# Performance work log

Hardware: AMD Instinct MI355X
Metric: run time of the kernel (lower is better)

Reference implementation:

```python
import jax, jax.numpy as jnp
import numpy as np

B, T, E = 32, 2048, 1024

def setup_inputs() -> dict:
    key = jax.random.key(0)
    k1, k2, k3 = jax.random.split(key, 3)
    enc = jax.random.normal(k1, (B, T, E), dtype=jnp.float32)
    ctx = jax.random.normal(k2, (B, E), dtype=jnp.float32)
    W = jax.random.normal(k3, (E, E), dtype=jnp.float32) * 0.05
    b = jnp.zeros((1, E), dtype=jnp.float32)
    return {"enc": enc, "ctx": ctx, "W": W, "b": b}

def reference(enc, ctx, W, b):
    # ht: (B, T, E) = tanh(enc @ W + b)
    ht = jnp.tanh(jnp.einsum('bte,ef->btf', enc, W) + b)
    # scores: (B, T) = batch dot of ctx against each timestep of ht
    scores = jnp.einsum('be,bte->bt', ctx, ht)
    at = jax.nn.softmax(scores, axis=-1)
    # weighted sum pooling over time -> (B, E)
    return jnp.einsum('bt,bte->be', at, ht)
```

## Files before the change

kernel.cpp:

```cpp
#include <hip/hip_runtime.h>
#include <hip/hip_bf16.h>
#include <math.h>

typedef unsigned short u16;
typedef unsigned int   u32;
typedef _Float16 f16x8 __attribute__((ext_vector_type(8)));
typedef float f32x4  __attribute__((ext_vector_type(4)));

#define Bb 32
#define Tt 2048
#define Ee 1024
#define Mm (Bb*Tt)
#define LSTR 40

__device__ __forceinline__ float tanh_fast(float x) {
  float ax = fminf(fabsf(x), 15.0f);
  float e  = __expf(2.0f * ax);
  float t  = 1.0f - 2.0f / (e + 1.0f);
  return copysignf(t, x);
}

__device__ __forceinline__ u32 pack2h(float a, float b) {
  _Float16 ha = (_Float16)a, hb = (_Float16)b;
  return (u32)__builtin_bit_cast(u16, ha) | ((u32)__builtin_bit_cast(u16, hb) << 16);
}

__global__ __launch_bounds__(256) void wt_convert(const float* __restrict__ W,
                                                  u16* __restrict__ Wt_hi,
                                                  u16* __restrict__ Wt_lo) {
  __shared__ float tile[32][33];
  int n0 = blockIdx.x * 32, k0 = blockIdx.y * 32;
  int tx = threadIdx.x, ty = threadIdx.y;
#pragma unroll
  for (int i = 0; i < 4; ++i)
    tile[ty + 8*i][tx] = W[(size_t)(k0 + ty + 8*i) * Ee + n0 + tx];
  __syncthreads();
#pragma unroll
  for (int i = 0; i < 4; ++i) {
    float v = tile[tx][ty + 8*i];
    _Float16 hi = (_Float16)v;
    float rem = v - (float)hi;
    _Float16 lo = (_Float16)rem;
    size_t idx = (size_t)(n0 + ty + 8*i) * Ee + k0 + tx;
    Wt_hi[idx] = __builtin_bit_cast(u16, hi);
    Wt_lo[idx] = __builtin_bit_cast(u16, lo);
  }
}

__global__ __launch_bounds__(256, 2) void gemm_tanh_score(
    const float* __restrict__ enc, const float* __restrict__ ctx,
    const float* __restrict__ bias,
    const u16* __restrict__ Wt_hi, const u16* __restrict__ Wt_lo,
    u16* __restrict__ ht, float* __restrict__ scores) {
  __shared__ u16 Ahf[128*LSTR], Bhi[128*LSTR], Blo[128*LSTR];

  int bx = blockIdx.x;
  int nt = bx & 7, mt = bx >> 3;
  int m0 = mt * 128, n0 = nt * 128;
  int tid = threadIdx.x;
  int w = tid >> 6, lane = tid & 63;
  int wm = (w & 1) * 64, wn = (w >> 1) * 64;
  int q = lane >> 4, c = lane & 15;

  f32x4 zero = {0.f, 0.f, 0.f, 0.f};
  f32x4 acc[4][4];
#pragma unroll
  for (int i = 0; i < 4; ++i)
#pragma unroll
    for (int j = 0; j < 4; ++j) acc[i][j] = zero;

  int ar = tid >> 1, ah = tid & 1;
  const float* Ap  = enc   + (size_t)(m0 + ar) * Ee + ah * 16;
  const u16*   BhP = Wt_hi + (size_t)(n0 + ar) * Ee + ah * 16;
  const u16*   BlP = Wt_lo + (size_t)(n0 + ar) * Ee + ah * 16;
  u16* AW  = &Ahf[ar * LSTR + ah * 16];
  u16* BhW = &Bhi[ar * LSTR + ah * 16];
  u16* BlW = &Blo[ar * LSTR + ah * 16];

  for (int kt = 0; kt < 32; ++kt) {
    const float4* ap = (const float4*)(Ap + (size_t)kt * 32);
    float4 f0 = ap[0], f1 = ap[1], f2 = ap[2], f3 = ap[3];
    const uint4* bhp = (const uint4*)(BhP + (size_t)kt * 32);
    uint4 bH0 = bhp[0], bH1 = bhp[1];
    const uint4* blp = (const uint4*)(BlP + (size_t)kt * 32);
    uint4 bL0 = blp[0], bL1 = blp[1];

    u32 a01 = pack2h(f0.x, f0.y), a23 = pack2h(f0.z, f0.w);
    u32 a45 = pack2h(f1.x, f1.y), a67 = pack2h(f1.z, f1.w);
    u32 a89 = pack2h(f2.x, f2.y), aAB = pack2h(f2.z, f2.w);
    u32 aCD = pack2h(f3.x, f3.y), aEF = pack2h(f3.z, f3.w);

    __syncthreads();
    ((uint4*)AW)[0]  = make_uint4(a01, a23, a45, a67);
    ((uint4*)AW)[1]  = make_uint4(a89, aAB, aCD, aEF);
    ((uint4*)BhW)[0] = bH0; ((uint4*)BhW)[1] = bH1;
    ((uint4*)BlW)[0] = bL0; ((uint4*)BlW)[1] = bL1;
    __syncthreads();

    f16x8 aF[4], bH[4], bL[4];
#pragma unroll
    for (int i = 0; i < 4; ++i) {
      int rax = (wm + i * 16 + c) * LSTR + q * 8;
      aF[i] = *(const f16x8*)(&Ahf[rax]);
      int rbx = (wn + i * 16 + c) * LSTR + q * 8;
      bH[i] = *(const f16x8*)(&Bhi[rbx]);
      bL[i] = *(const f16x8*)(&Blo[rbx]);
    }
#pragma unroll
    for (int i = 0; i < 4; ++i)
#pragma unroll
      for (int j = 0; j < 4; ++j) {
        acc[i][j] = __builtin_amdgcn_mfma_f32_16x16x32_f16(aF[i], bH[j], acc[i][j], 0, 0, 0);
        acc[i][j] = __builtin_amdgcn_mfma_f32_16x16x32_f16(aF[i], bL[j], acc[i][j], 0, 0, 0);
      }
  }

  int bidx = m0 >> 11;
  float ctxv[4], biasv[4];
#pragma unroll
  for (int j = 0; j < 4; ++j) {
    int col = n0 + wn + j * 16 + c;
    ctxv[j]  = ctx[bidx * Ee + col];
    biasv[j] = bias[col];
  }
#pragma unroll
  for (int i = 0; i < 4; ++i) {
#pragma unroll
    for (int r = 0; r < 4; ++r) {
      int rowG = m0 + wm + i * 16 + q * 4 + r;
      u16* hrow = ht + (size_t)rowG * Ee + n0 + wn + c;
      float s = 0.f;
#pragma unroll
      for (int j = 0; j < 4; ++j) {
        float h = tanh_fast(acc[i][j][r] + biasv[j]);
        __hip_bfloat16 hb = __float2bfloat16(h);
        hrow[j * 16] = *(u16*)&hb;
        s += h * ctxv[j];
      }
      s += __shfl_xor(s, 1); s += __shfl_xor(s, 2);
      s += __shfl_xor(s, 4); s += __shfl_xor(s, 8);
      if (c == 0) atomicAdd(&scores[rowG], s);
    }
  }
}

__global__ __launch_bounds__(256) void softmax_t(const float* __restrict__ scores,
                                                 float* __restrict__ at) {
  __shared__ float red[256];
  int b = blockIdx.x, tid = threadIdx.x;
  float v[8];
  float mx = -3.0e38f;
#pragma unroll
  for (int i = 0; i < 8; ++i) {
    v[i] = scores[b * Tt + i * 256 + tid];
    mx = fmaxf(mx, v[i]);
  }
  red[tid] = mx; __syncthreads();
  for (int s = 128; s > 0; s >>= 1) {
    if (tid < s) red[tid] = fmaxf(red[tid], red[tid + s]);
    __syncthreads();
  }
  mx = red[0]; __syncthreads();
  float sum = 0.f;
#pragma unroll
  for (int i = 0; i < 8; ++i) { v[i] = __expf(v[i] - mx); sum += v[i]; }
  red[tid] = sum; __syncthreads();
  for (int s = 128; s > 0; s >>= 1) {
    if (tid < s) red[tid] += red[tid + s];
    __syncthreads();
  }
  float inv = 1.0f / red[0];
#pragma unroll
  for (int i = 0; i < 8; ++i) at[b * Tt + i * 256 + tid] = v[i] * inv;
}

__global__ __launch_bounds__(256) void weighted_sum(const u16* __restrict__ ht,
                                                    const float* __restrict__ at,
                                                    float* __restrict__ part) {
  __shared__ float ats[64];
  int bx = blockIdx.x;
  int b = bx >> 5, tc = bx & 31;
  int tid = threadIdx.x;
  if (tid < 64) ats[tid] = at[b * Tt + tc * 64 + tid];
  __syncthreads();
  int e0 = tid * 4;
  const u16* base = ht + (size_t)(b * Tt + tc * 64) * Ee + e0;
  float s0 = 0.f, s1 = 0.f, s2 = 0.f, s3 = 0.f;
#pragma unroll 4
  for (int t = 0; t < 64; ++t) {
    float a = ats[t];
    uint2 u = *(const uint2*)(base + (size_t)t * Ee);
    s0 += a * __uint_as_float(u.x << 16);
    s1 += a * __uint_as_float(u.x & 0xffff0000u);
    s2 += a * __uint_as_float(u.y << 16);
    s3 += a * __uint_as_float(u.y & 0xffff0000u);
  }
  float4 out4 = make_float4(s0, s1, s2, s3);
  *(float4*)(part + ((size_t)(b * 32 + tc) * Ee + e0)) = out4;
}

__global__ __launch_bounds__(256) void reduce_part(const float* __restrict__ part,
                                                   float* __restrict__ out) {
  int b = blockIdx.x, tid = threadIdx.x;
  float4 s = make_float4(0.f, 0.f, 0.f, 0.f);
#pragma unroll
  for (int tc = 0; tc < 32; ++tc) {
    float4 p = ((const float4*)(part + (size_t)(b * 32 + tc) * Ee))[tid];
    s.x += p.x; s.y += p.y; s.z += p.z; s.w += p.w;
  }
  ((float4*)(out + (size_t)b * Ee))[tid] = s;
}

extern "C" void kernel_launch(void* const* d_in, const int* in_sizes, int n_in,
                              void* d_out, int out_size, void* d_ws, size_t ws_size,
                              hipStream_t stream) {
  const float* enc  = (const float*)d_in[0];
  const float* ctx  = (const float*)d_in[1];
  const float* W    = (const float*)d_in[2];
  const float* bias = (const float*)d_in[3];
  float* out = (float*)d_out;

  char* ws = (char*)d_ws;
  u16* Wt_hi = (u16*)(ws);
  u16* Wt_lo = (u16*)(ws + (size_t)2 * 1024 * 1024);
  u16* ht    = (u16*)(ws + (size_t)4 * 1024 * 1024);
  float* scores = (float*)(ws + (size_t)4 * 1024 * 1024 + (size_t)Mm * Ee * 2);
  float* at     = scores + Mm;
  float* part   = (float*)ws;

  hipMemsetAsync(scores, 0, (size_t)Mm * sizeof(float), stream);

  wt_convert<<<dim3(32, 32), dim3(32, 8), 0, stream>>>(W, Wt_hi, Wt_lo);
  gemm_tanh_score<<<dim3(4096), dim3(256), 0, stream>>>(enc, ctx, bias, Wt_hi, Wt_lo, ht, scores);
  softmax_t<<<dim3(32), dim3(256), 0, stream>>>(scores, at);
  weighted_sum<<<dim3(1024), dim3(256), 0, stream>>>(ht, at, part);
  reduce_part<<<dim3(32), dim3(256), 0, stream>>>(part, out);
}
```

Measured before the change: 716.5 us.

## Prefetch next K-tile into registers, swizzle block order, store ht as fp16

The GEMM main loop now loads the next K-tile of enc and W halves into registers right after the shared-memory store, so global latency overlaps the MFMA work on the current tile. Block indices are remapped so groups of 8 consecutive blocks cover different M tiles across all N tiles, which changes L2 reuse of enc and W. The ht intermediate moves from bf16 to fp16, giving it more mantissa precision at the cost of a smaller range, though tanh output stays within [-1,1]. The register prefetch raises register pressure under launch_bounds(256,2).

```diff
diff --git a/kernel.cpp b/kernel.cpp
--- a/kernel.cpp
+++ b/kernel.cpp
@@ -55,7 +55,9 @@
   __shared__ u16 Ahf[128*LSTR], Bhi[128*LSTR], Blo[128*LSTR];
 
   int bx = blockIdx.x;
-  int nt = bx & 7, mt = bx >> 3;
+  int x = bx & 7, local = bx >> 3;
+  int nt = local & 7;
+  int mt = ((local >> 3) << 3) + x;
   int m0 = mt * 128, n0 = nt * 128;
   int tid = threadIdx.x;
   int w = tid >> 6, lane = tid & 63;
@@ -77,25 +79,39 @@
   u16* BhW = &Bhi[ar * LSTR + ah * 16];
   u16* BlW = &Blo[ar * LSTR + ah * 16];
 
+  float4 fA0, fA1, fA2, fA3;
+  uint4 vH0, vH1, vL0, vL1;
+  {
+    const float4* ap = (const float4*)Ap;
+    fA0 = ap[0]; fA1 = ap[1]; fA2 = ap[2]; fA3 = ap[3];
+    const uint4* bhp = (const uint4*)BhP;
+    vH0 = bhp[0]; vH1 = bhp[1];
+    const uint4* blp = (const uint4*)BlP;
+    vL0 = blp[0]; vL1 = blp[1];
+  }
+
   for (int kt = 0; kt < 32; ++kt) {
-    const float4* ap = (const float4*)(Ap + (size_t)kt * 32);
-    float4 f0 = ap[0], f1 = ap[1], f2 = ap[2], f3 = ap[3];
-    const uint4* bhp = (const uint4*)(BhP + (size_t)kt * 32);
-    uint4 bH0 = bhp[0], bH1 = bhp[1];
-    const uint4* blp = (const uint4*)(BlP + (size_t)kt * 32);
-    uint4 bL0 = blp[0], bL1 = blp[1];
-
-    u32 a01 = pack2h(f0.x, f0.y), a23 = pack2h(f0.z, f0.w);
-    u32 a45 = pack2h(f1.x, f1.y), a67 = pack2h(f1.z, f1.w);
-    u32 a89 = pack2h(f2.x, f2.y), aAB = pack2h(f2.z, f2.w);
-    u32 aCD = pack2h(f3.x, f3.y), aEF = pack2h(f3.z, f3.w);
+    u32 a01 = pack2h(fA0.x, fA0.y), a23 = pack2h(fA0.z, fA0.w);
+    u32 a45 = pack2h(fA1.x, fA1.y), a67 = pack2h(fA1.z, fA1.w);
+    u32 a89 = pack2h(fA2.x, fA2.y), aAB = pack2h(fA2.z, fA2.w);
+    u32 aCD = pack2h(fA3.x, fA3.y), aEF = pack2h(fA3.z, fA3.w);
 
     __syncthreads();
     ((uint4*)AW)[0]  = make_uint4(a01, a23, a45, a67);
     ((uint4*)AW)[1]  = make_uint4(a89, aAB, aCD, aEF);
-    ((uint4*)BhW)[0] = bH0; ((uint4*)BhW)[1] = bH1;
-    ((uint4*)BlW)[0] = bL0; ((uint4*)BlW)[1] = bL1;
-    __syncthreads();
+    ((uint4*)BhW)[0] = vH0; ((uint4*)BhW)[1] = vH1;
+    ((uint4*)BlW)[0] = vL0; ((uint4*)BlW)[1] = vL1;
+    __syncthreads();
+
+    {
+      int kt2 = (kt < 31) ? kt + 1 : 31;
+      const float4* ap = (const float4*)(Ap + (size_t)kt2 * 32);
+      fA0 = ap[0]; fA1 = ap[1]; fA2 = ap[2]; fA3 = ap[3];
+      const uint4* bhp = (const uint4*)(BhP + (size_t)kt2 * 32);
+      vH0 = bhp[0]; vH1 = bhp[1];
+      const uint4* blp = (const uint4*)(BlP + (size_t)kt2 * 32);
+      vL0 = blp[0]; vL1 = blp[1];
+    }
 
     f16x8 aF[4], bH[4], bL[4];
 #pragma unroll
@@ -133,8 +149,8 @@
 #pragma unroll
       for (int j = 0; j < 4; ++j) {
         float h = tanh_fast(acc[i][j][r] + biasv[j]);
-        __hip_bfloat16 hb = __float2bfloat16(h);
-        hrow[j * 16] = *(u16*)&hb;
+        _Float16 hf = (_Float16)h;
+        hrow[j * 16] = __builtin_bit_cast(u16, hf);
         s += h * ctxv[j];
       }
       s += __shfl_xor(s, 1); s += __shfl_xor(s, 2);
@@ -190,10 +206,10 @@
   for (int t = 0; t < 64; ++t) {
     float a = ats[t];
     uint2 u = *(const uint2*)(base + (size_t)t * Ee);
-    s0 += a * __uint_as_float(u.x << 16);
-    s1 += a * __uint_as_float(u.x & 0xffff0000u);
-    s2 += a * __uint_as_float(u.y << 16);
-    s3 += a * __uint_as_float(u.y & 0xffff0000u);
+    s0 += a * (float)__builtin_bit_cast(_Float16, (u16)(u.x & 0xffff));
+    s1 += a * (float)__builtin_bit_cast(_Float16, (u16)(u.x >> 16));
+    s2 += a * (float)__builtin_bit_cast(_Float16, (u16)(u.y & 0xffff));
+    s3 += a * (float)__builtin_bit_cast(_Float16, (u16)(u.y >> 16));
   }
   float4 out4 = make_float4(s0, s1, s2, s3);
   *(float4*)(part + ((size_t)(b * 32 + tc) * Ee + e0)) = out4;
```

After: 730.1 us. About the same (+1.9%).

## Pre-convert enc to fp16 and stream GEMM tiles via direct global-to-LDS loads

Applied to the files above, without the earlier changes.

Adds a separate pass that converts enc to fp16 in workspace. The GEMM then fills its LDS tiles with global_load_lds DMA instead of register staging and conversion, using unpadded 32-wide rows. Block indices are also swizzled so neighbouring blocks share enc rows for L2 reuse, and ht is stored as fp16 instead of bf16. The trade is an extra full read and write of enc (256MB fp32 in, 128MB fp16 out) against fewer GEMM instructions and registers; unpadded LDS rows risk bank conflicts. The old path is kept when the workspace is too small.

```diff
diff --git a/kernel.cpp b/kernel.cpp
--- a/kernel.cpp
+++ b/kernel.cpp
@@ -11,7 +11,6 @@
 #define Tt 2048
 #define Ee 1024
 #define Mm (Bb*Tt)
-#define LSTR 40
 
 __device__ __forceinline__ float tanh_fast(float x) {
   float ax = fminf(fabsf(x), 15.0f);
@@ -23,6 +22,27 @@
 __device__ __forceinline__ u32 pack2h(float a, float b) {
   _Float16 ha = (_Float16)a, hb = (_Float16)b;
   return (u32)__builtin_bit_cast(u16, ha) | ((u32)__builtin_bit_cast(u16, hb) << 16);
+}
+
+__device__ __forceinline__ void glb2lds16(const u16* g, u16* l) {
+  __builtin_amdgcn_global_load_lds(
+      (const __attribute__((address_space(1))) void*)g,
+      (__attribute__((address_space(3))) void*)l, 16, 0, 0);
+}
+
+__global__ __launch_bounds__(256) void enc_convert(const float* __restrict__ enc,
+                                                   u16* __restrict__ enc16) {
+  size_t t = (size_t)blockIdx.x * 256 + threadIdx.x;
+  const size_t stride = (size_t)2048 * 256;
+#pragma unroll 2
+  for (int s = 0; s < 16; ++s) {
+    size_t g = (s * stride + t) * 8;
+    const float4* p = (const float4*)(enc + g);
+    float4 f0 = p[0], f1 = p[1];
+    uint4 o = make_uint4(pack2h(f0.x, f0.y), pack2h(f0.z, f0.w),
+                         pack2h(f1.x, f1.y), pack2h(f1.z, f1.w));
+    *(uint4*)(enc16 + g) = o;
+  }
 }
 
 __global__ __launch_bounds__(256) void wt_convert(const float* __restrict__ W,
@@ -47,7 +67,104 @@
   }
 }
 
-__global__ __launch_bounds__(256, 2) void gemm_tanh_score(
+__global__ __launch_bounds__(256, 2) void gemm_dma(
+    const u16* __restrict__ enc16, const float* __restrict__ ctx,
+    const float* __restrict__ bias,
+    const u16* __restrict__ Wt_hi, const u16* __restrict__ Wt_lo,
+    u16* __restrict__ ht, float* __restrict__ scores) {
+  __shared__ u16 Ah[4096], Bh[4096], Bl[4096];
+
+  int bx = blockIdx.x;
+  int x = bx & 7, local = bx >> 3;
+  int nt = local & 7;
+  int mt = ((local >> 3) << 3) + x;
+  int m0 = mt * 128, n0 = nt * 128;
+  int tid = threadIdx.x;
+  int w = tid >> 6, lane = tid & 63;
+  int wm = (w & 1) * 64, wn = (w >> 1) * 64;
+  int q = lane >> 4, c = lane & 15;
+
+  f32x4 zero = {0.f, 0.f, 0.f, 0.f};
+  f32x4 acc[4][4];
+#pragma unroll
+  for (int i = 0; i < 4; ++i)
+#pragma unroll
+    for (int j = 0; j < 4; ++j) acc[i][j] = zero;
+
+  int r0 = (0 * 4 + w) * 16 + (lane >> 2);
+  int r1 = (1 * 4 + w) * 16 + (lane >> 2);
+  int kc = (lane & 3) * 8;
+  const u16* gA0 = enc16 + (size_t)(m0 + r0) * Ee + kc;
+  const u16* gA1 = enc16 + (size_t)(m0 + r1) * Ee + kc;
+  const u16* gH0 = Wt_hi + (size_t)(n0 + r0) * Ee + kc;
+  const u16* gH1 = Wt_hi + (size_t)(n0 + r1) * Ee + kc;
+  const u16* gL0 = Wt_lo + (size_t)(n0 + r0) * Ee + kc;
+  const u16* gL1 = Wt_lo + (size_t)(n0 + r1) * Ee + kc;
+  u16* lA0 = &Ah[(0 * 4 + w) * 512 + lane * 8];
+  u16* lA1 = &Ah[(1 * 4 + w) * 512 + lane * 8];
+  u16* lH0 = &Bh[(0 * 4 + w) * 512 + lane * 8];
+  u16* lH1 = &Bh[(1 * 4 + w) * 512 + lane * 8];
+  u16* lL0 = &Bl[(0 * 4 + w) * 512 + lane * 8];
+  u16* lL1 = &Bl[(1 * 4 + w) * 512 + lane * 8];
+
+  for (int kt = 0; kt < 32; ++kt) {
+    __syncthreads();
+    int ko = kt * 32;
+    glb2lds16(gA0 + ko, lA0);
+    glb2lds16(gA1 + ko, lA1);
+    glb2lds16(gH0 + ko, lH0);
+    glb2lds16(gH1 + ko, lH1);
+    glb2lds16(gL0 + ko, lL0);
+    glb2lds16(gL1 + ko, lL1);
+    __syncthreads();
+
+    f16x8 aF[4], bH[4], bL[4];
+#pragma unroll
+    for (int i = 0; i < 4; ++i) {
+      aF[i] = *(const f16x8*)(&Ah[(wm + i * 16 + c) * 32 + q * 8]);
+      bH[i] = *(const f16x8*)(&Bh[(wn + i * 16 + c) * 32 + q * 8]);
+      bL[i] = *(const f16x8*)(&Bl[(wn + i * 16 + c) * 32 + q * 8]);
+    }
+#pragma unroll
+    for (int i = 0; i < 4; ++i)
+#pragma unroll
+      for (int j = 0; j < 4; ++j) {
+        acc[i][j] = __builtin_amdgcn_mfma_f32_16x16x32_f16(aF[i], bH[j], acc[i][j], 0, 0, 0);
+        acc[i][j] = __builtin_amdgcn_mfma_f32_16x16x32_f16(aF[i], bL[j], acc[i][j], 0, 0, 0);
+      }
+  }
+
+  int bidx = m0 >> 11;
+  float ctxv[4], biasv[4];
+#pragma unroll
+  for (int j = 0; j < 4; ++j) {
+    int col = n0 + wn + j * 16 + c;
+    ctxv[j]  = ctx[bidx * Ee + col];
+    biasv[j] = bias[col];
+  }
+#pragma unroll
+  for (int i = 0; i < 4; ++i) {
+#pragma unroll
+    for (int r = 0; r < 4; ++r) {
+      int rowG = m0 + wm + i * 16 + q * 4 + r;
+      u16* hrow = ht + (size_t)rowG * Ee + n0 + wn + c;
+      float s = 0.f;
+#pragma unroll
+      for (int j = 0; j < 4; ++j) {
+        float h = tanh_fast(acc[i][j][r] + biasv[j]);
+        _Float16 hf = (_Float16)h;
+        hrow[j * 16] = __builtin_bit_cast(u16, hf);
+        s += h * ctxv[j];
+      }
+      s += __shfl_xor(s, 1); s += __shfl_xor(s, 2);
+      s += __shfl_xor(s, 4); s += __shfl_xor(s, 8);
+      if (c == 0) atomicAdd(&scores[rowG], s);
+    }
+  }
+}
+
+#define LSTR 40
+__global__ __launch_bounds__(256, 2) void gemm_reg(
     const float* __restrict__ enc, const float* __restrict__ ctx,
     const float* __restrict__ bias,
     const u16* __restrict__ Wt_hi, const u16* __restrict__ Wt_lo,
@@ -55,7 +172,9 @@
   __shared__ u16 Ahf[128*LSTR], Bhi[128*LSTR], Blo[128*LSTR];
 
   int bx = blockIdx.x;
-  int nt = bx & 7, mt = bx >> 3;
+  int x = bx & 7, local = bx >> 3;
+  int nt = local & 7;
+  int mt = ((local >> 3) << 3) + x;
   int m0 = mt * 128, n0 = nt * 128;
   int tid = threadIdx.x;
   int w = tid >> 6, lane = tid & 63;
@@ -100,11 +219,9 @@
     f16x8 aF[4], bH[4], bL[4];
 #pragma unroll
     for (int i = 0; i < 4; ++i) {
-      int rax = (wm + i * 16 + c) * LSTR + q * 8;
-      aF[i] = *(const f16x8*)(&Ahf[rax]);
-      int rbx = (wn + i * 16 + c) * LSTR + q * 8;
-      bH[i] = *(const f16x8*)(&Bhi[rbx]);
-      bL[i] = *(const f16x8*)(&Blo[rbx]);
+      aF[i] = *(const f16x8*)(&Ahf[(wm + i * 16 + c) * LSTR + q * 8]);
+      bH[i] = *(const f16x8*)(&Bhi[(wn + i * 16 + c) * LSTR + q * 8]);
+      bL[i] = *(const f16x8*)(&Blo[(wn + i * 16 + c) * LSTR + q * 8]);
     }
 #pragma unroll
     for (int i = 0; i < 4; ++i)
@@ -133,8 +250,8 @@
 #pragma unroll
       for (int j = 0; j < 4; ++j) {
         float h = tanh_fast(acc[i][j][r] + biasv[j]);
-        __hip_bfloat16 hb = __float2bfloat16(h);
-        hrow[j * 16] = *(u16*)&hb;
+        _Float16 hf = (_Float16)h;
+        hrow[j * 16] = __builtin_bit_cast(u16, hf);
         s += h * ctxv[j];
       }
       s += __shfl_xor(s, 1); s += __shfl_xor(s, 2);
@@ -190,13 +307,12 @@
   for (int t = 0; t < 64; ++t) {
     float a = ats[t];
     uint2 u = *(const uint2*)(base + (size_t)t * Ee);
-    s0 += a * __uint_as_float(u.x << 16);
-    s1 += a * __uint_as_float(u.x & 0xffff0000u);
-    s2 += a * __uint_as_float(u.y << 16);
-    s3 += a * __uint_as_float(u.y & 0xffff0000u);
-  }
-  float4 out4 = make_float4(s0, s1, s2, s3);
-  *(float4*)(part + ((size_t)(b * 32 + tc) * Ee + e0)) = out4;
+    s0 += a * (float)__builtin_bit_cast(_Float16, (u16)(u.x & 0xffff));
+    s1 += a * (float)__builtin_bit_cast(_Float16, (u16)(u.x >> 16));
+    s2 += a * (float)__builtin_bit_cast(_Float16, (u16)(u.y & 0xffff));
+    s3 += a * (float)__builtin_bit_cast(_Float16, (u16)(u.y >> 16));
+  }
+  *(float4*)(part + ((size_t)(b * 32 + tc) * Ee + e0)) = make_float4(s0, s1, s2, s3);
 }
 
 __global__ __launch_bounds__(256) void reduce_part(const float* __restrict__ part,
@@ -221,17 +337,33 @@
   float* out = (float*)d_out;
 
   char* ws = (char*)d_ws;
+  const size_t MB = 1024 * 1024;
   u16* Wt_hi = (u16*)(ws);
-  u16* Wt_lo = (u16*)(ws + (size_t)2 * 1024 * 1024);
-  u16* ht    = (u16*)(ws + (size_t)4 * 1024 * 1024);
-  float* scores = (float*)(ws + (size_t)4 * 1024 * 1024 + (size_t)Mm * Ee * 2);
-  float* at     = scores + Mm;
-  float* part   = (float*)ws;
+  u16* Wt_lo = (u16*)(ws + 2 * MB);
+  float* part = (float*)ws;
+
+  bool dma = ws_size >= 262 * MB;
+  u16* enc16; u16* ht; float* scores; float* at;
+  if (dma) {
+    enc16  = (u16*)(ws + 4 * MB);
+    ht     = (u16*)(ws + 132 * MB);
+    scores = (float*)(ws + 260 * MB);
+  } else {
+    enc16  = nullptr;
+    ht     = (u16*)(ws + 4 * MB);
+    scores = (float*)(ws + 132 * MB);
+  }
+  at = scores + Mm;
 
   hipMemsetAsync(scores, 0, (size_t)Mm * sizeof(float), stream);
 
   wt_convert<<<dim3(32, 32), dim3(32, 8), 0, stream>>>(W, Wt_hi, Wt_lo);
-  gemm_tanh_score<<<dim3(4096), dim3(256), 0, stream>>>(enc, ctx, bias, Wt_hi, Wt_lo, ht, scores);
+  if (dma) {
+    enc_convert<<<dim3(2048), dim3(256), 0, stream>>>(enc, enc16);
+    gemm_dma<<<dim3(4096), dim3(256), 0, stream>>>(enc16, ctx, bias, Wt_hi, Wt_lo, ht, scores);
+  } else {
+    gemm_reg<<<dim3(4096), dim3(256), 0, stream>>>(enc, ctx, bias, Wt_hi, Wt_lo, ht, scores);
+  }
   softmax_t<<<dim3(32), dim3(256), 0, stream>>>(scores, at);
   weighted_sum<<<dim3(1024), dim3(256), 0, stream>>>(ht, at, part);
   reduce_part<<<dim3(32), dim3(256), 0, stream>>>(part, out);
```

After: 730.4 us. No clear change (+1.9%).
